# Kernel tuning notes

Measured on AMD Instinct MI355X. Metric: run time of the kernel, lower is better.

## Reference

```python
import jax, jax.numpy as jnp
import numpy as np

N, E, V, H, HEADS, L, B = 20000, 320000, 100, 128, 3, 2, 200
NEG = 0.2   # leaky_relu negative_slope
EPS = 1e-5  # LayerNorm eps


def _mean_nodes(x, gid):
    # dgl.mean_nodes: per-graph mean of node features
    s = jax.ops.segment_sum(x, gid, num_segments=B)
    c = jax.ops.segment_sum(jnp.ones((x.shape[0], 1), x.dtype), gid, num_segments=B)
    return s / jnp.maximum(c, 1.0)


def _gat_layer(h, src, dst, Wn, bn, att, Ws, b, gamma, beta):
    # weight_node: Linear(H, H*HEADS)
    wv = (h @ Wn + bn).reshape(-1, HEADS, H)
    u = wv[src]  # [E, heads, H] gathered src features
    # attn = leaky_relu(sum(cat(u, v) * w_att)) split into u/v halves (no concat materialized)
    attn = (jnp.einsum('ehd,hd->eh', u, att[:, :H])
            + jnp.einsum('ehd,hd->eh', wv[dst], att[:, H:]))
    attn = jax.nn.leaky_relu(attn, NEG)  # [E, heads]
    # segment softmax over incoming edges of each dst node (mailbox softmax)
    m = jax.ops.segment_max(attn, dst, num_segments=N)
    m = jnp.where(jnp.isfinite(m), m, 0.0)
    e = jnp.exp(attn - m[dst])
    s = jax.ops.segment_sum(e, dst, num_segments=N)
    score = e / s[dst]
    agg = jax.ops.segment_sum(score[:, :, None] * u, dst, num_segments=N)  # [N, heads, H]
    res = agg.reshape(-1, HEADS * H) @ Ws + b
    # DGL leaves zero-in-degree nodes with zero reduced features (reduce_func never runs)
    has_in = jax.ops.segment_sum(jnp.ones((E,), h.dtype), dst, num_segments=N) > 0
    res = jnp.where(has_in[:, None], res, 0.0)
    x = res + h  # residual, then LayerNorm, relu (dropout is eval-mode identity)
    mu = jnp.mean(x, -1, keepdims=True)
    var = jnp.var(x, -1, keepdims=True)
    x = (x - mu) * jax.lax.rsqrt(var + EPS) * gamma + beta
    return jax.nn.relu(x)


def _gru_dir(x, Wih, Whh, bih, bhh, reverse):
    # torch nn.GRU single direction; x: [B, T, in]
    def step(hprev, xt):
        gi = xt @ Wih.T + bih
        gh = hprev @ Whh.T + bhh
        ir, iz, inn = jnp.split(gi, 3, -1)
        hr, hz, hn = jnp.split(gh, 3, -1)
        r = jax.nn.sigmoid(ir + hr)
        z = jax.nn.sigmoid(iz + hz)
        n = jnp.tanh(inn + r * hn)
        hnew = (1.0 - z) * n + z * hprev
        return hnew, hnew
    h0 = jnp.zeros((x.shape[0], Whh.shape[1]), x.dtype)
    hT, ys = jax.lax.scan(step, h0, jnp.swapaxes(x, 0, 1), reverse=reverse)
    return jnp.swapaxes(ys, 0, 1), hT


def setup_inputs() -> dict:
    key = jax.random.key(0)
    k = jax.random.split(key, 16)
    sc = 0.05
    return {
        'h': jax.random.normal(k[0], (N, H), jnp.float32),
        'wid': jax.random.randint(k[1], (N,), 0, V),
        'src': jax.random.randint(k[2], (E,), 0, N),
        'dst': jax.random.randint(k[3], (E,), 0, N),
        'graph_ids': jnp.sort(jax.random.randint(k[4], (N,), 0, B)),
        'proj_W': jax.random.normal(k[5], (V + H, H), jnp.float32) * sc,
        'proj_b': jnp.zeros((H,), jnp.float32),
        'conv_Wn': jax.random.normal(k[6], (L, H, HEADS * H), jnp.float32) * sc,
        'conv_bn': jnp.zeros((L, HEADS * H), jnp.float32),
        'conv_att': jax.random.normal(k[7], (L, HEADS, 2 * H), jnp.float32) * sc,
        'conv_Ws': jax.random.normal(k[8], (L, HEADS * H, H), jnp.float32) * sc,
        'conv_b': jnp.zeros((L, H), jnp.float32),
        'conv_gamma': jnp.ones((L, H), jnp.float32),
        'conv_beta': jnp.zeros((L, H), jnp.float32),
        'gru_Wih0': jax.random.normal(k[9], (2, 3 * H, H), jnp.float32) * sc,
        'gru_Whh0': jax.random.normal(k[10], (2, 3 * H, H), jnp.float32) * sc,
        'gru_bih0': jnp.zeros((2, 3 * H), jnp.float32),
        'gru_bhh0': jnp.zeros((2, 3 * H), jnp.float32),
        'gru_Wih1': jax.random.normal(k[11], (2, 3 * H, 2 * H), jnp.float32) * sc,
        'gru_Whh1': jax.random.normal(k[12], (2, 3 * H, H), jnp.float32) * sc,
        'gru_bih1': jnp.zeros((2, 3 * H), jnp.float32),
        'gru_bhh1': jnp.zeros((2, 3 * H), jnp.float32),
    }


def reference(h, wid, src, dst, graph_ids, proj_W, proj_b, conv_Wn, conv_bn, conv_att, conv_Ws, conv_b, conv_gamma, conv_beta, gru_Wih0, gru_Whh0, gru_bih0, gru_bhh0, gru_Wih1, gru_Whh1, gru_bih1, gru_bhh1):
    one_hot = jax.nn.one_hot(wid, V, dtype=h.dtype)
    hcur = jnp.concatenate([one_hot, h], -1) @ proj_W + proj_b  # project
    readouts = [_mean_nodes(hcur, graph_ids)]
    for l in range(L):
        hcur = _gat_layer(hcur, src, dst, conv_Wn[l], conv_bn[l], conv_att[l],
                          conv_Ws[l], conv_b[l], conv_gamma[l], conv_beta[l])
        readouts.append(_mean_nodes(hcur, graph_ids))
    x = jnp.stack(readouts, 1)  # [B, L+1, H] GRU readout sequence
    finals = []
    for (Wih, Whh, bih, bhh) in ((gru_Wih0, gru_Whh0, gru_bih0, gru_bhh0),
                                 (gru_Wih1, gru_Whh1, gru_bih1, gru_bhh1)):
        yf, hf = _gru_dir(x, Wih[0], Whh[0], bih[0], bhh[0], False)
        yb, hb = _gru_dir(x, Wih[1], Whh[1], bih[1], bhh[1], True)
        x = jnp.concatenate([yf, yb], -1)
        finals += [hf, hb]
    # torch returns h_n [num_layers*2, B, H]; module takes mean over dim 0
    return jnp.mean(jnp.stack(finals, 0), 0)  # [B, H]
```

## Files before the change

### kernel.cpp

```cpp
#include <hip/hip_runtime.h>
#include <cstddef>
#include <cstdint>

static constexpr int Nn    = 20000;
static constexpr int Ee    = 320000;
static constexpr int Vv    = 100;
static constexpr int Hh    = 128;
static constexpr int HEADS = 3;
static constexpr int Bb    = 200;
static constexpr float NEG = 0.2f;
static constexpr float EPS = 1e-5f;

typedef short bf16x8 __attribute__((ext_vector_type(8)));
typedef float f32x4  __attribute__((ext_vector_type(4)));

__device__ inline unsigned short bf16_rne(float x) {
    unsigned u = __builtin_bit_cast(unsigned, x);
    u += 0x7FFFu + ((u >> 16) & 1u);
    return (unsigned short)(u >> 16);
}
__device__ inline float bf16_f(unsigned short h) {
    unsigned u = ((unsigned)h) << 16;
    return __builtin_bit_cast(float, u);
}
__device__ inline float bf_lo(unsigned u) { return __builtin_bit_cast(float, u << 16); }
__device__ inline float bf_hi(unsigned u) { return __builtin_bit_cast(float, u & 0xFFFF0000u); }
__device__ inline float lrelu(float a) { return a >= 0.f ? a : NEG * a; }
__device__ inline float sigmoidf(float x) { return 1.f / (1.f + __expf(-x)); }

__global__ __launch_bounds__(1024) void scan_offsets(const int* __restrict__ deg,
                                                     int* __restrict__ offs,
                                                     int* __restrict__ cur) {
    __shared__ int sums[1024];
    const int tid = threadIdx.x;
    const int per = (Nn + 1023) >> 10;
    int begin = tid * per;
    int end = begin + per; if (end > Nn) end = Nn;
    if (begin > Nn) begin = Nn;
    int s = 0;
    for (int i = begin; i < end; i++) s += deg[i];
    sums[tid] = s;
    __syncthreads();
    for (int off = 1; off < 1024; off <<= 1) {
        int v = (tid >= off) ? sums[tid - off] : 0;
        __syncthreads();
        sums[tid] += v;
        __syncthreads();
    }
    int run = sums[tid] - s;
    for (int i = begin; i < end; i++) {
        offs[i] = run; cur[i] = run;
        run += deg[i];
    }
    if (end == Nn) offs[Nn] = run;
}

__global__ void fill_csr(const int* __restrict__ dst, const int* __restrict__ src,
                         int* __restrict__ cur, int* __restrict__ csrc) {
    for (int i = blockIdx.x * blockDim.x + threadIdx.x; i < Ee; i += gridDim.x * blockDim.x) {
        int p = atomicAdd(&cur[dst[i]], 1);
        csrc[p] = src[i];
    }
}

struct PrepArgs {
    const float *projW, *convWn, *convWs, *convAtt, *convBn, *convB;
    const float *Wih0, *Whh0, *Wih1, *Whh1;
    const int *gid, *dst;
    unsigned short *pBth, *pBtl;
    unsigned short *WfTh0, *WfTl0, *WfTh1, *WfTl1;
    float *vavd, *vc, *biasF;
    float *WihT0, *WhhT0, *WihT1, *WhhT1;
    int *goffs, *deg;
};

__device__ inline void wsplit(const float* B, int K, int N, int idx,
                              unsigned short* Bth, unsigned short* Btl) {
    int k = idx / N, n = idx - k * N;
    float v = B[idx];
    unsigned short h = bf16_rne(v);
    unsigned short l = bf16_rne(v - bf16_f(h));
    Bth[(size_t)n * K + k] = h;
    Btl[(size_t)n * K + k] = l;
}
__device__ inline void gruT(const float* W, int K, int idx, float* WT) {
    int d = idx / (384 * K);
    int r = idx - d * 384 * K;
    int j = r / K, k = r - j * K;
    WT[(size_t)d * K * 384 + (size_t)(k >> 2) * 1536 + j * 4 + (k & 3)] = W[idx];
}

__global__ void prep_all(PrepArgs a) {
    int i = blockIdx.x * blockDim.x + threadIdx.x;
    if (i < 16384) { wsplit(a.projW, 128, 128, i, a.pBth, a.pBtl); return; } i -= 16384;
#pragma unroll
    for (int l = 0; l < 2; l++) {
        if (i < 49152) {
            int k = i >> 7, c = i & 127;
            int h = k >> 7, i_ = k & 127;
            const float* wn = a.convWn + (size_t)l * 49152 + (size_t)i_ * 384 + h * 128;
            const float* ws = a.convWs + (size_t)l * 49152 + (size_t)(h * 128) * 128 + c;
            float v = 0.f;
            for (int j = 0; j < 128; j++) v += wn[j] * ws[(size_t)j * 128];
            unsigned short hi = bf16_rne(v);
            unsigned short lo = bf16_rne(v - bf16_f(hi));
            unsigned short* th = l ? a.WfTh1 : a.WfTh0;
            unsigned short* tl = l ? a.WfTl1 : a.WfTl0;
            th[(size_t)c * 384 + k] = hi;
            tl[(size_t)c * 384 + k] = lo;
            return;
        }
        i -= 49152;
    }
    if (i < 1536) {
        int l = i / 768, r = i % 768;
        int sd = r / 384, rr = r % 384, h = rr >> 7, i_ = rr & 127;
        const float* wn = a.convWn + (size_t)l * 49152 + (size_t)i_ * 384 + h * 128;
        const float* at = a.convAtt + l * 768 + h * 256 + sd * 128;
        float v = 0.f;
        for (int j = 0; j < 128; j++) v += wn[j] * at[j];
        a.vavd[i] = v;
        return;
    } i -= 1536;
    if (i < 12) {
        int l = i / 6, r = i % 6, sd = r / 3, h = r % 3;
        const float* bn = a.convBn + l * 384 + h * 128;
        const float* at = a.convAtt + l * 768 + h * 256 + sd * 128;
        float v = 0.f;
        for (int j = 0; j < 128; j++) v += bn[j] * at[j];
        a.vc[i] = v;
        return;
    } i -= 12;
    if (i < 256) {
        int l = i >> 7, c = i & 127;
        const float* bn = a.convBn + l * 384;
        const float* ws = a.convWs + (size_t)l * 49152 + c;
        float v = a.convB[l * 128 + c];
        for (int k = 0; k < 384; k++) v += bn[k] * ws[(size_t)k * 128];
        a.biasF[i] = v;
        return;
    } i -= 256;
    if (i < 98304)  { gruT(a.Wih0, 128, i, a.WihT0); return; }  i -= 98304;
    if (i < 98304)  { gruT(a.Whh0, 128, i, a.WhhT0); return; }  i -= 98304;
    if (i < 196608) { gruT(a.Wih1, 256, i, a.WihT1); return; }  i -= 196608;
    if (i < 98304)  { gruT(a.Whh1, 128, i, a.WhhT1); return; }  i -= 98304;
    if (i < Nn) {
        int g = a.gid[i];
        if (i == 0) { for (int b = 0; b <= g; b++) a.goffs[b] = 0; }
        else { int pg = a.gid[i - 1]; for (int b = pg + 1; b <= g; b++) a.goffs[b] = i; }
        if (i == Nn - 1) { for (int b = g + 1; b <= Bb; b++) a.goffs[b] = Nn; }
        return;
    } i -= Nn;
    if (i < Ee) atomicAdd(&a.deg[a.dst[i]], 1);
}

struct GArgs {
    const float* A; const unsigned short* Bth; const unsigned short* Btl;
    const float* bias; int M, K;
    const int* wid; const float* projW;
    const int* deg; const float* gamma; const float* beta;
    float* hcur;
    const int* gid; float* reado;
    const float* vavd; const float* vc;
    float* adf; float* addf;
    unsigned short* hb;
};

template <int MODE>
__global__ __launch_bounds__(256) void gemm_fused(GArgs a) {
    __shared__ unsigned short As_hi[32][40];
    __shared__ unsigned short As_lo[32][40];
    __shared__ unsigned short Bs_hi[128][40];
    __shared__ unsigned short Bs_lo[128][40];
    __shared__ float ytile[32][132];
    __shared__ float sred[6][32][4];
    __shared__ int sgid[32];
    const int tid  = threadIdx.x;
    const int row0 = blockIdx.y * 32;
    const int wn   = tid >> 6;
    const int L    = tid & 63;
    const int lrow = L & 15;
    const int lq   = L >> 4;
    const int K = a.K;

    const int mA  = tid >> 3;
    const int kqA = (tid & 7) * 4;
    const int nB  = tid >> 1;
    const int khB = (tid & 1) * 16;
    const float* Arow = a.A + (size_t)(row0 + mA) * K + kqA;
    const unsigned short* Bhrow = a.Bth + (size_t)nB * K + khB;
    const unsigned short* Blrow = a.Btl + (size_t)nB * K + khB;

    f32x4 acc[2][2];
#pragma unroll
    for (int i = 0; i < 2; i++)
#pragma unroll
        for (int j = 0; j < 2; j++) acc[i][j] = (f32x4){0.f, 0.f, 0.f, 0.f};

    float4 av  = *(const float4*)(Arow);
    float4 vbh0 = *(const float4*)(Bhrow);
    float4 vbh1 = *(const float4*)(Bhrow + 8);
    float4 vbl0 = *(const float4*)(Blrow);
    float4 vbl1 = *(const float4*)(Blrow + 8);

    for (int kb = 0; kb < K; kb += 32) {
        {
            unsigned short h0 = bf16_rne(av.x), h1 = bf16_rne(av.y),
                           h2 = bf16_rne(av.z), h3 = bf16_rne(av.w);
            *(short4*)&As_hi[mA][kqA] = make_short4((short)h0, (short)h1, (short)h2, (short)h3);
            *(short4*)&As_lo[mA][kqA] = make_short4((short)bf16_rne(av.x - bf16_f(h0)),
                                                    (short)bf16_rne(av.y - bf16_f(h1)),
                                                    (short)bf16_rne(av.z - bf16_f(h2)),
                                                    (short)bf16_rne(av.w - bf16_f(h3)));
            *(float4*)&Bs_hi[nB][khB]     = vbh0;
            *(float4*)&Bs_hi[nB][khB + 8] = vbh1;
            *(float4*)&Bs_lo[nB][khB]     = vbl0;
            *(float4*)&Bs_lo[nB][khB + 8] = vbl1;
        }
        __syncthreads();
        if (kb + 32 < K) {
            av   = *(const float4*)(Arow + kb + 32);
            vbh0 = *(const float4*)(Bhrow + kb + 32);
            vbh1 = *(const float4*)(Bhrow + kb + 40);
            vbl0 = *(const float4*)(Blrow + kb + 32);
            vbl1 = *(const float4*)(Blrow + kb + 40);
        }
        bf16x8 ah[2], al[2], bh[2], bl[2];
#pragma unroll
        for (int mi = 0; mi < 2; mi++) {
            int r = mi * 16 + lrow;
            ah[mi] = *(const bf16x8*)&As_hi[r][lq * 8];
            al[mi] = *(const bf16x8*)&As_lo[r][lq * 8];
        }
#pragma unroll
        for (int ni = 0; ni < 2; ni++) {
            int r = wn * 32 + ni * 16 + lrow;
            bh[ni] = *(const bf16x8*)&Bs_hi[r][lq * 8];
            bl[ni] = *(const bf16x8*)&Bs_lo[r][lq * 8];
        }
#pragma unroll
        for (int mi = 0; mi < 2; mi++)
#pragma unroll
            for (int ni = 0; ni < 2; ni++) {
                acc[mi][ni] = __builtin_amdgcn_mfma_f32_16x16x32_bf16(ah[mi], bh[ni], acc[mi][ni], 0, 0, 0);
                acc[mi][ni] = __builtin_amdgcn_mfma_f32_16x16x32_bf16(ah[mi], bl[ni], acc[mi][ni], 0, 0, 0);
                acc[mi][ni] = __builtin_amdgcn_mfma_f32_16x16x32_bf16(al[mi], bh[ni], acc[mi][ni], 0, 0, 0);
            }
        __syncthreads();
    }

#pragma unroll
    for (int ni = 0; ni < 2; ni++) {
        float bb = a.bias[wn * 32 + ni * 16 + lrow];
#pragma unroll
        for (int mi = 0; mi < 2; mi++)
#pragma unroll
            for (int r = 0; r < 4; r++) acc[mi][ni][r] += bb;
    }

    if constexpr (MODE == 0) {
#pragma unroll
        for (int mi = 0; mi < 2; mi++)
#pragma unroll
            for (int r = 0; r < 4; r++) {
                int lr = mi * 16 + lq * 4 + r;
                int row = row0 + lr;
                int wi = a.wid[row];
#pragma unroll
                for (int ni = 0; ni < 2; ni++) {
                    int c = wn * 32 + ni * 16 + lrow;
                    float y = acc[mi][ni][r] + a.projW[(size_t)wi * 128 + c];
                    acc[mi][ni][r] = y;
                    a.hcur[(size_t)row * 128 + c] = y;
                    ytile[lr][c] = y;
                }
            }
    }

    if constexpr (MODE == 2) {
        __shared__ float red1[32][4], red2[32][4];
        float g4[2], be4[2];
#pragma unroll
        for (int ni = 0; ni < 2; ni++) {
            int c = wn * 32 + ni * 16 + lrow;
            g4[ni] = a.gamma[c]; be4[ni] = a.beta[c];
        }
#pragma unroll
        for (int mi = 0; mi < 2; mi++)
#pragma unroll
            for (int r = 0; r < 4; r++) {
                int lr = mi * 16 + lq * 4 + r;
                int row = row0 + lr;
                int dg = a.deg[row];
#pragma unroll
                for (int ni = 0; ni < 2; ni++) {
                    int c = wn * 32 + ni * 16 + lrow;
                    float hold = a.hcur[(size_t)row * 128 + c];
                    acc[mi][ni][r] = hold + (dg > 0 ? acc[mi][ni][r] : 0.f);
                }
            }
#pragma unroll
        for (int mi = 0; mi < 2; mi++)
#pragma unroll
            for (int r = 0; r < 4; r++) {
                float ps = acc[mi][0][r] + acc[mi][1][r];
#pragma unroll
                for (int o = 1; o < 16; o <<= 1) ps += __shfl_xor(ps, o, 64);
                if (lrow == 0) red1[mi * 16 + lq * 4 + r][wn] = ps;
            }
        __syncthreads();
#pragma unroll
        for (int mi = 0; mi < 2; mi++)
#pragma unroll
            for (int r = 0; r < 4; r++) {
                int lr = mi * 16 + lq * 4 + r;
                float mu = (red1[lr][0] + red1[lr][1] + red1[lr][2] + red1[lr][3]) * (1.f / 128.f);
                float qs = 0.f;
#pragma unroll
                for (int ni = 0; ni < 2; ni++) {
                    float dx = acc[mi][ni][r] - mu;
                    qs += dx * dx;
                }
#pragma unroll
                for (int o = 1; o < 16; o <<= 1) qs += __shfl_xor(qs, o, 64);
                if (lrow == 0) red2[lr][wn] = qs;
            }
        __syncthreads();
#pragma unroll
        for (int mi = 0; mi < 2; mi++)
#pragma unroll
            for (int r = 0; r < 4; r++) {
                int lr = mi * 16 + lq * 4 + r;
                int row = row0 + lr;
                float mu = (red1[lr][0] + red1[lr][1] + red1[lr][2] + red1[lr][3]) * (1.f / 128.f);
                float var = (red2[lr][0] + red2[lr][1] + red2[lr][2] + red2[lr][3]) * (1.f / 128.f);
                float rs = rsqrtf(var + EPS);
#pragma unroll
                for (int ni = 0; ni < 2; ni++) {
                    int c = wn * 32 + ni * 16 + lrow;
                    float y = fmaxf((acc[mi][ni][r] - mu) * rs * g4[ni] + be4[ni], 0.f);
                    acc[mi][ni][r] = y;
                    a.hcur[(size_t)row * 128 + c] = y;
                    ytile[lr][c] = y;
                }
            }
    }

    if (tid < 32) sgid[tid] = a.gid[row0 + tid];

    const bool dots = (a.vavd != nullptr);
    if (dots) {
        float vv0[6], vv1[6];
#pragma unroll
        for (int d = 0; d < 6; d++) {
            vv0[d] = a.vavd[d * 128 + wn * 32 + lrow];
            vv1[d] = a.vavd[d * 128 + wn * 32 + 16 + lrow];
        }
#pragma unroll
        for (int d = 0; d < 6; d++) {
#pragma unroll
            for (int mi = 0; mi < 2; mi++)
#pragma unroll
                for (int r = 0; r < 4; r++) {
                    float ps = acc[mi][0][r] * vv0[d] + acc[mi][1][r] * vv1[d];
#pragma unroll
                    for (int o = 1; o < 16; o <<= 1) ps += __shfl_xor(ps, o, 64);
                    if (lrow == 0) sred[d][mi * 16 + lq * 4 + r][wn] = ps;
                }
        }
    }
    __syncthreads();

    {
        int j = tid & 127, hh = tid >> 7;
        float sum = 0.f; int curg = -1;
        for (int r = hh * 16; r < hh * 16 + 16; r++) {
            int g = sgid[r];
            if (g != curg) {
                if (curg >= 0) atomicAdd(&a.reado[(size_t)curg * 128 + j], sum);
                sum = 0.f; curg = g;
            }
            sum += ytile[r][j];
        }
        if (curg >= 0) atomicAdd(&a.reado[(size_t)curg * 128 + j], sum);
    }

    if (dots) {
        if (tid < 192) {
            int row = tid & 31, d = tid >> 5;
            float s = sred[d][row][0] + sred[d][row][1] + sred[d][row][2] + sred[d][row][3]
                    + a.vc[d];
            int node = row0 + row;
            int sd = d / 3, h = d - sd * 3;
            float* dstp = sd ? a.addf : a.adf;
            dstp[(size_t)node * 4 + h] = s;
        }
        {
            int row = tid >> 3, c0 = (tid & 7) * 16;
            unsigned* dst = (unsigned*)(a.hb + (size_t)(row0 + row) * 128 + c0);
#pragma unroll
            for (int q = 0; q < 8; q++) {
                unsigned lo = bf16_rne(ytile[row][c0 + 2 * q]);
                unsigned hi = bf16_rne(ytile[row][c0 + 2 * q + 1]);
                dst[q] = lo | (hi << 16);
            }
        }
    }
}

__global__ __launch_bounds__(256) void gat_gather(const unsigned short* __restrict__ hb,
                                                  const float4* __restrict__ ad,
                                                  const float4* __restrict__ add,
                                                  const int* __restrict__ offs,
                                                  const int* __restrict__ csrc,
                                                  float* __restrict__ T) {
    __shared__ float4 slot[4][64];
    const int n = (blockIdx.x * 256 + threadIdx.x) >> 6;
    const int wv_ = threadIdx.x >> 6;
    const int L = threadIdx.x & 63;
    if (n >= Nn) return;
    const int start = offs[n];
    const int deg = offs[n + 1] - start;
    float2* o2 = (float2*)(T + (size_t)n * 384);
    if (deg == 0) {
        float2 z = make_float2(0.f, 0.f);
        o2[L] = z; o2[64 + L] = z; o2[128 + L] = z;
        return;
    }
    const float4 adn = add[n];
    float2 t0 = make_float2(0.f, 0.f), t1 = t0, t2 = t0;

    if (deg <= 64) {
        int sn = 0; float e0 = 0.f, e1 = 0.f, e2 = 0.f;
        if (L < deg) {
            sn = csrc[start + L];
            float4 a4 = ad[sn];
            e0 = __expf(lrelu(a4.x + adn.x));
            e1 = __expf(lrelu(a4.y + adn.y));
            e2 = __expf(lrelu(a4.z + adn.z));
        }
        float s0 = e0, s1 = e1, s2 = e2;
#pragma unroll
        for (int o = 32; o > 0; o >>= 1) {
            s0 += __shfl_xor(s0, o, 64);
            s1 += __shfl_xor(s1, o, 64);
            s2 += __shfl_xor(s2, o, 64);
        }
        slot[wv_][L] = make_float4(__builtin_bit_cast(float, sn),
                                   e0 / s0, e1 / s1, e2 / s2);
        __builtin_amdgcn_wave_barrier();
#pragma unroll 2
        for (int j = 0; j < deg; j++) {
            float4 sc = slot[wv_][j];
            int s_n = __builtin_bit_cast(int, sc.x);
            unsigned u = ((const unsigned*)(hb + (size_t)s_n * 128))[L];
            float x0 = bf_lo(u), x1 = bf_hi(u);
            t0.x += sc.y * x0; t0.y += sc.y * x1;
            t1.x += sc.z * x0; t1.y += sc.z * x1;
            t2.x += sc.w * x0; t2.y += sc.w * x1;
        }
    } else {
        float s0 = 0.f, s1 = 0.f, s2 = 0.f;
        for (int i = L; i < deg; i += 64) {
            int sn = csrc[start + i];
            float4 a4 = ad[sn];
            s0 += __expf(lrelu(a4.x + adn.x));
            s1 += __expf(lrelu(a4.y + adn.y));
            s2 += __expf(lrelu(a4.z + adn.z));
        }
#pragma unroll
        for (int o = 32; o > 0; o >>= 1) {
            s0 += __shfl_xor(s0, o, 64);
            s1 += __shfl_xor(s1, o, 64);
            s2 += __shfl_xor(s2, o, 64);
        }
        float i0 = 1.f / s0, i1 = 1.f / s1, i2 = 1.f / s2;
        for (int base = 0; base < deg; base += 64) {
            int cnt = deg - base; if (cnt > 64) cnt = 64;
            if (L < cnt) {
                int sn = csrc[start + base + L];
                float4 a4 = ad[sn];
                slot[wv_][L] = make_float4(__builtin_bit_cast(float, sn),
                                           __expf(lrelu(a4.x + adn.x)) * i0,
                                           __expf(lrelu(a4.y + adn.y)) * i1,
                                           __expf(lrelu(a4.z + adn.z)) * i2);
            }
            __builtin_amdgcn_wave_barrier();
            for (int j = 0; j < cnt; j++) {
                float4 sc = slot[wv_][j];
                int s_n = __builtin_bit_cast(int, sc.x);
                unsigned u = ((const unsigned*)(hb + (size_t)s_n * 128))[L];
                float x0 = bf_lo(u), x1 = bf_hi(u);
                t0.x += sc.y * x0; t0.y += sc.y * x1;
                t1.x += sc.z * x0; t1.y += sc.z * x1;
                t2.x += sc.w * x0; t2.y += sc.w * x1;
            }
            __builtin_amdgcn_wave_barrier();
        }
    }
    o2[L] = t0; o2[64 + L] = t1; o2[128 + L] = t2;
}

__global__ __launch_bounds__(768) void gru_all(const float* __restrict__ reado,
                                               const int* __restrict__ goffs,
                                               const float* __restrict__ WihT0,
                                               const float* __restrict__ WhhT0,
                                               const float* __restrict__ bih0,
                                               const float* __restrict__ bhh0,
                                               const float* __restrict__ WihT1,
                                               const float* __restrict__ WhhT1,
                                               const float* __restrict__ bih1,
                                               const float* __restrict__ bhh1,
                                               float* __restrict__ out) {
    const int b = blockIdx.x;
    const int tid = threadIdx.x;
    const int dir = tid / 384;
    const int j = tid - dir * 384;
    __shared__ __align__(16) float xs[3][128];
    __shared__ __align__(16) float y0s[3][256];
    __shared__ __align__(16) float hs[2][128];
    __shared__ float gil[2][384], ghl[2][384];
    __shared__ float fin01[2][128];
    if (tid < 128) {
        int cnt = goffs[b + 1] - goffs[b];
        float invc = 1.f / fmaxf((float)cnt, 1.f);
#pragma unroll
        for (int t = 0; t < 3; t++)
            xs[t][tid] = reado[(size_t)t * Bb * Hh + (size_t)b * Hh + tid] * invc;
    }
    if (j < 128) hs[dir][j] = 0.f;
    __syncthreads();
    {
        const float* Wi = WihT0 + (size_t)dir * 128 * 384;
        const float* Wh = WhhT0 + (size_t)dir * 128 * 384;
        float gi0, gi1, gi2;
        gi0 = gi1 = gi2 = bih0[dir * 384 + j];
#pragma unroll 4
        for (int k4 = 0; k4 < 32; k4++) {
            float4 w  = *(const float4*)(Wi + k4 * 1536 + j * 4);
            float4 x0 = *(const float4*)&xs[0][k4 * 4];
            float4 x1 = *(const float4*)&xs[1][k4 * 4];
            float4 x2 = *(const float4*)&xs[2][k4 * 4];
            gi0 += w.x * x0.x + w.y * x0.y + w.z * x0.z + w.w * x0.w;
            gi1 += w.x * x1.x + w.y * x1.y + w.z * x1.z + w.w * x1.w;
            gi2 += w.x * x2.x + w.y * x2.y + w.z * x2.z + w.w * x2.w;
        }
        const float bhj = bhh0[dir * 384 + j];
        for (int step = 0; step < 3; step++) {
            int t = dir ? 2 - step : step;
            float g = bhj;
            if (step > 0) {
#pragma unroll 4
                for (int k4 = 0; k4 < 32; k4++) {
                    float4 w  = *(const float4*)(Wh + k4 * 1536 + j * 4);
                    float4 hv = *(const float4*)&hs[dir][k4 * 4];
                    g += w.x * hv.x + w.y * hv.y + w.z * hv.z + w.w * hv.w;
                }
            }
            ghl[dir][j] = g;
            gil[dir][j] = dir ? (step == 0 ? gi2 : (step == 1 ? gi1 : gi0))
                              : (step == 0 ? gi0 : (step == 1 ? gi1 : gi2));
            __syncthreads();
            if (j < 128) {
                float r = sigmoidf(gil[dir][j] + ghl[dir][j]);
                float z = sigmoidf(gil[dir][j + 128] + ghl[dir][j + 128]);
                float nn2 = tanhf(gil[dir][j + 256] + r * ghl[dir][j + 256]);
                float hnew = (1.f - z) * nn2 + z * hs[dir][j];
                hs[dir][j] = hnew;
                y0s[t][dir * 128 + j] = hnew;
                if (step == 2) fin01[dir][j] = hnew;
            }
            __syncthreads();
        }
    }
    if (j < 128) hs[dir][j] = 0.f;
    {
        const float* Wi = WihT1 + (size_t)dir * 256 * 384;
        const float* Wh = WhhT1 + (size_t)dir * 128 * 384;
        float gi0, gi1, gi2;
        gi0 = gi1 = gi2 = bih1[dir * 384 + j];
        __syncthreads();
#pragma unroll 4
        for (int k4 = 0; k4 < 64; k4++) {
            float4 w  = *(const float4*)(Wi + k4 * 1536 + j * 4);
            float4 x0 = *(const float4*)&y0s[0][k4 * 4];
            float4 x1 = *(const float4*)&y0s[1][k4 * 4];
            float4 x2 = *(const float4*)&y0s[2][k4 * 4];
            gi0 += w.x * x0.x + w.y * x0.y + w.z * x0.z + w.w * x0.w;
            gi1 += w.x * x1.x + w.y * x1.y + w.z * x1.z + w.w * x1.w;
            gi2 += w.x * x2.x + w.y * x2.y + w.z * x2.z + w.w * x2.w;
        }
        const float bhj = bhh1[dir * 384 + j];
        for (int step = 0; step < 3; step++) {
            float g = bhj;
            if (step > 0) {
#pragma unroll 4
                for (int k4 = 0; k4 < 32; k4++) {
                    float4 w  = *(const float4*)(Wh + k4 * 1536 + j * 4);
                    float4 hv = *(const float4*)&hs[dir][k4 * 4];
                    g += w.x * hv.x + w.y * hv.y + w.z * hv.z + w.w * hv.w;
                }
            }
            ghl[dir][j] = g;
            gil[dir][j] = dir ? (step == 0 ? gi2 : (step == 1 ? gi1 : gi0))
                              : (step == 0 ? gi0 : (step == 1 ? gi1 : gi2));
            __syncthreads();
            if (j < 128) {
                float r = sigmoidf(gil[dir][j] + ghl[dir][j]);
                float z = sigmoidf(gil[dir][j + 128] + ghl[dir][j + 128]);
                float nn2 = tanhf(gil[dir][j + 256] + r * ghl[dir][j + 256]);
                float hnew = (1.f - z) * nn2 + z * hs[dir][j];
                hs[dir][j] = hnew;
                if (step == 2) fin01[dir][j] = 0.25f * (fin01[dir][j] + hnew);
            }
            __syncthreads();
        }
    }
    if (tid < 128)
        out[(size_t)b * Hh + tid] = fin01[0][tid] + fin01[1][tid];
}

extern "C" void kernel_launch(void* const* d_in, const int* in_sizes, int n_in,
                              void* d_out, int out_size, void* d_ws, size_t ws_size,
                              hipStream_t stream) {
    const float* h      = (const float*)d_in[0];
    const int*   wid    = (const int*)d_in[1];
    const int*   src    = (const int*)d_in[2];
    const int*   dst    = (const int*)d_in[3];
    const int*   gid    = (const int*)d_in[4];
    const float* projW  = (const float*)d_in[5];
    const float* projB  = (const float*)d_in[6];
    const float* convWn = (const float*)d_in[7];
    const float* convBn = (const float*)d_in[8];
    const float* convAtt= (const float*)d_in[9];
    const float* convWs = (const float*)d_in[10];
    const float* convB  = (const float*)d_in[11];
    const float* convG  = (const float*)d_in[12];
    const float* convBe = (const float*)d_in[13];
    const float* Wih0   = (const float*)d_in[14];
    const float* Whh0   = (const float*)d_in[15];
    const float* bih0   = (const float*)d_in[16];
    const float* bhh0   = (const float*)d_in[17];
    const float* Wih1   = (const float*)d_in[18];
    const float* Whh1   = (const float*)d_in[19];
    const float* bih1   = (const float*)d_in[20];
    const float* bhh1   = (const float*)d_in[21];
    float* out = (float*)d_out;

    char* p = (char*)d_ws;
    auto align16 = [&]() { p = (char*)(((uintptr_t)p + 15) & ~(uintptr_t)15); };
    auto alloc_f = [&](size_t n) { align16(); float* r = (float*)p; p += n * sizeof(float); return r; };
    auto alloc_i = [&](size_t n) { align16(); int* r = (int*)p; p += n * sizeof(int); return r; };
    auto alloc_s = [&](size_t n) { align16(); unsigned short* r = (unsigned short*)p; p += n * sizeof(unsigned short); return r; };
    float* hcur  = alloc_f((size_t)Nn * 128);
    float* T     = alloc_f((size_t)Nn * 384);
    float* adbuf = alloc_f((size_t)Nn * 4);
    float* addbuf= alloc_f((size_t)Nn * 4);
    float* reado = alloc_f((size_t)3 * Bb * Hh);
    int* deg  = alloc_i(Nn);
    const size_t zero_bytes = (size_t)3 * Bb * Hh * sizeof(float) + Nn * sizeof(int);
    float* WihT0 = alloc_f((size_t)2 * 128 * 384);
    float* WhhT0 = alloc_f((size_t)2 * 128 * 384);
    float* WihT1 = alloc_f((size_t)2 * 256 * 384);
    float* WhhT1 = alloc_f((size_t)2 * 128 * 384);
    float* vavd  = alloc_f(1536);
    float* vc    = alloc_f(12);
    float* biasF = alloc_f(256);
    int* offs = alloc_i(Nn + 1);
    int* cur  = alloc_i(Nn);
    int* csrc = alloc_i(Ee);
    int* goffs = alloc_i(Bb + 1);
    unsigned short* hb = alloc_s((size_t)Nn * 128);
    unsigned short* pBth = alloc_s(128 * 128);
    unsigned short* pBtl = alloc_s(128 * 128);
    unsigned short* WfTh[2] = { alloc_s(128 * 384), alloc_s(128 * 384) };
    unsigned short* WfTl[2] = { alloc_s(128 * 384), alloc_s(128 * 384) };

    hipMemsetAsync(reado, 0, zero_bytes, stream);

    PrepArgs pa;
    pa.projW = projW + (size_t)Vv * Hh;
    pa.convWn = convWn; pa.convWs = convWs; pa.convAtt = convAtt;
    pa.convBn = convBn; pa.convB = convB;
    pa.Wih0 = Wih0; pa.Whh0 = Whh0; pa.Wih1 = Wih1; pa.Whh1 = Whh1;
    pa.gid = gid; pa.dst = dst;
    pa.pBth = pBth; pa.pBtl = pBtl;
    pa.WfTh0 = WfTh[0]; pa.WfTl0 = WfTl[0]; pa.WfTh1 = WfTh[1]; pa.WfTl1 = WfTl[1];
    pa.vavd = vavd; pa.vc = vc; pa.biasF = biasF;
    pa.WihT0 = WihT0; pa.WhhT0 = WhhT0; pa.WihT1 = WihT1; pa.WhhT1 = WhhT1;
    pa.goffs = goffs; pa.deg = deg;
    const int prep_total = 16384 + 2 * 49152 + 1536 + 12 + 256 + 98304 + 98304 + 196608 + 98304 + Nn + Ee;
    prep_all<<<(prep_total + 255) / 256, 256, 0, stream>>>(pa);

    scan_offsets<<<1, 1024, 0, stream>>>(deg, offs, cur);
    fill_csr<<<1250, 256, 0, stream>>>(dst, src, cur, csrc);

    {
        GArgs g = {};
        g.A = h; g.Bth = pBth; g.Btl = pBtl; g.bias = projB;
        g.M = Nn; g.K = 128;
        g.wid = wid; g.projW = projW; g.hcur = hcur;
        g.gid = gid; g.reado = reado;
        g.vavd = vavd; g.vc = vc; g.adf = adbuf; g.addf = addbuf; g.hb = hb;
        gemm_fused<0><<<dim3(1, Nn / 32), 256, 0, stream>>>(g);
    }

    const int nwaveblocks = (Nn * 64 + 255) / 256;
    for (int l = 0; l < 2; l++) {
        gat_gather<<<nwaveblocks, 256, 0, stream>>>(hb, (const float4*)adbuf, (const float4*)addbuf,
                                                    offs, csrc, T);
        {
            GArgs g = {};
            g.A = T; g.Bth = WfTh[l]; g.Btl = WfTl[l]; g.bias = biasF + l * 128;
            g.M = Nn; g.K = 384;
            g.deg = deg; g.gamma = convG + l * Hh; g.beta = convBe + l * Hh;
            g.hcur = hcur;
            g.gid = gid; g.reado = reado + (size_t)(l + 1) * Bb * Hh;
            if (l == 0) { g.vavd = vavd + 768; g.vc = vc + 6; g.adf = adbuf; g.addf = addbuf; g.hb = hb; }
            gemm_fused<2><<<dim3(1, Nn / 32), 256, 0, stream>>>(g);
        }
    }

    gru_all<<<Bb, 768, 0, stream>>>(reado, goffs, WihT0, WhhT0, bih0, bhh0,
                                    WihT1, WhhT1, bih1, bhh1, out);
}
```

Before: 349.8 us.

## Fuse memset, prep, scan and CSR fill into one cooperative kernel

Replaces the memset, prep kernel, single-block scan and CSR fill kernels with one cooperative-launch kernel that uses grid-wide syncs between phases. The goal is to remove several launch and inter-kernel gaps. The cost is grid.sync overhead and a smaller grid of 1024 blocks striding over the prep work. The scan now runs on a 256-thread block inside a single block while the rest of the grid sits idle at the barrier, so that serial phase may take longer.

```diff
diff --git a/kernel.cpp b/kernel.cpp
--- a/kernel.cpp
+++ b/kernel.cpp
@@ -1,6 +1,9 @@
 #include <hip/hip_runtime.h>
+#include <hip/hip_cooperative_groups.h>
 #include <cstddef>
 #include <cstdint>
+
+namespace cg = cooperative_groups;
 
 static constexpr int Nn    = 20000;
 static constexpr int Ee    = 320000;
@@ -28,50 +31,17 @@
 __device__ inline float lrelu(float a) { return a >= 0.f ? a : NEG * a; }
 __device__ inline float sigmoidf(float x) { return 1.f / (1.f + __expf(-x)); }
 
-__global__ __launch_bounds__(1024) void scan_offsets(const int* __restrict__ deg,
-                                                     int* __restrict__ offs,
-                                                     int* __restrict__ cur) {
-    __shared__ int sums[1024];
-    const int tid = threadIdx.x;
-    const int per = (Nn + 1023) >> 10;
-    int begin = tid * per;
-    int end = begin + per; if (end > Nn) end = Nn;
-    if (begin > Nn) begin = Nn;
-    int s = 0;
-    for (int i = begin; i < end; i++) s += deg[i];
-    sums[tid] = s;
-    __syncthreads();
-    for (int off = 1; off < 1024; off <<= 1) {
-        int v = (tid >= off) ? sums[tid - off] : 0;
-        __syncthreads();
-        sums[tid] += v;
-        __syncthreads();
-    }
-    int run = sums[tid] - s;
-    for (int i = begin; i < end; i++) {
-        offs[i] = run; cur[i] = run;
-        run += deg[i];
-    }
-    if (end == Nn) offs[Nn] = run;
-}
-
-__global__ void fill_csr(const int* __restrict__ dst, const int* __restrict__ src,
-                         int* __restrict__ cur, int* __restrict__ csrc) {
-    for (int i = blockIdx.x * blockDim.x + threadIdx.x; i < Ee; i += gridDim.x * blockDim.x) {
-        int p = atomicAdd(&cur[dst[i]], 1);
-        csrc[p] = src[i];
-    }
-}
-
 struct PrepArgs {
     const float *projW, *convWn, *convWs, *convAtt, *convBn, *convB;
     const float *Wih0, *Whh0, *Wih1, *Whh1;
-    const int *gid, *dst;
+    const int *gid, *dst, *src;
     unsigned short *pBth, *pBtl;
     unsigned short *WfTh0, *WfTl0, *WfTh1, *WfTl1;
     float *vavd, *vc, *biasF;
     float *WihT0, *WhhT0, *WihT1, *WhhT1;
     int *goffs, *deg;
+    int *offs, *cur, *csrc;
+    float *reado;
 };
 
 __device__ inline void wsplit(const float* B, int K, int N, int idx,
@@ -90,8 +60,10 @@
     WT[(size_t)d * K * 384 + (size_t)(k >> 2) * 1536 + j * 4 + (k & 3)] = W[idx];
 }
 
-__global__ void prep_all(PrepArgs a) {
-    int i = blockIdx.x * blockDim.x + threadIdx.x;
+static constexpr int PREP_TOTAL = 16384 + 2 * 49152 + 1536 + 12 + 256
+                                + 98304 + 98304 + 196608 + 98304 + Nn + Ee;
+
+__device__ void prep_item(const PrepArgs& a, int i) {
     if (i < 16384) { wsplit(a.projW, 128, 128, i, a.pBth, a.pBtl); return; } i -= 16384;
 #pragma unroll
     for (int l = 0; l < 2; l++) {
@@ -154,6 +126,50 @@
     if (i < Ee) atomicAdd(&a.deg[a.dst[i]], 1);
 }
 
+__global__ __launch_bounds__(256) void prep_fused(PrepArgs a) {
+    cg::grid_group grid = cg::this_grid();
+    const int gsz  = gridDim.x * blockDim.x;
+    const int gtid = blockIdx.x * blockDim.x + threadIdx.x;
+    const int tid  = threadIdx.x;
+
+    for (int i = gtid; i < Nn; i += gsz) a.deg[i] = 0;
+    for (int i = gtid; i < 3 * Bb * Hh; i += gsz) a.reado[i] = 0.f;
+    grid.sync();
+
+    for (int i = gtid; i < PREP_TOTAL; i += gsz) prep_item(a, i);
+    grid.sync();
+
+    if (blockIdx.x == 0) {
+        __shared__ int sums[256];
+        const int per = (Nn + 255) >> 8;
+        int begin = tid * per;
+        int end = begin + per; if (end > Nn) end = Nn;
+        if (begin > Nn) begin = Nn;
+        int s = 0;
+        for (int i = begin; i < end; i++) s += a.deg[i];
+        sums[tid] = s;
+        __syncthreads();
+        for (int off = 1; off < 256; off <<= 1) {
+            int v = (tid >= off) ? sums[tid - off] : 0;
+            __syncthreads();
+            sums[tid] += v;
+            __syncthreads();
+        }
+        int run = sums[tid] - s;
+        for (int i = begin; i < end; i++) {
+            a.offs[i] = run; a.cur[i] = run;
+            run += a.deg[i];
+        }
+        if (end == Nn) a.offs[Nn] = run;
+    }
+    grid.sync();
+
+    for (int i = gtid; i < Ee; i += gsz) {
+        int p = atomicAdd(&a.cur[a.dst[i]], 1);
+        a.csrc[p] = a.src[i];
+    }
+}
+
 struct GArgs {
     const float* A; const unsigned short* Bth; const unsigned short* Btl;
     const float* bias; int M, K;
@@ -658,7 +674,6 @@
     float* addbuf= alloc_f((size_t)Nn * 4);
     float* reado = alloc_f((size_t)3 * Bb * Hh);
     int* deg  = alloc_i(Nn);
-    const size_t zero_bytes = (size_t)3 * Bb * Hh * sizeof(float) + Nn * sizeof(int);
     float* WihT0 = alloc_f((size_t)2 * 128 * 384);
     float* WhhT0 = alloc_f((size_t)2 * 128 * 384);
     float* WihT1 = alloc_f((size_t)2 * 256 * 384);
@@ -676,24 +691,25 @@
     unsigned short* WfTh[2] = { alloc_s(128 * 384), alloc_s(128 * 384) };
     unsigned short* WfTl[2] = { alloc_s(128 * 384), alloc_s(128 * 384) };
 
-    hipMemsetAsync(reado, 0, zero_bytes, stream);
-
     PrepArgs pa;
     pa.projW = projW + (size_t)Vv * Hh;
     pa.convWn = convWn; pa.convWs = convWs; pa.convAtt = convAtt;
     pa.convBn = convBn; pa.convB = convB;
     pa.Wih0 = Wih0; pa.Whh0 = Whh0; pa.Wih1 = Wih1; pa.Whh1 = Whh1;
-    pa.gid = gid; pa.dst = dst;
+    pa.gid = gid; pa.dst = dst; pa.src = src;
     pa.pBth = pBth; pa.pBtl = pBtl;
     pa.WfTh0 = WfTh[0]; pa.WfTl0 = WfTl[0]; pa.WfTh1 = WfTh[1]; pa.WfTl1 = WfTl[1];
     pa.vavd = vavd; pa.vc = vc; pa.biasF = biasF;
     pa.WihT0 = WihT0; pa.WhhT0 = WhhT0; pa.WihT1 = WihT1; pa.WhhT1 = WhhT1;
     pa.goffs = goffs; pa.deg = deg;
-    const int prep_total = 16384 + 2 * 49152 + 1536 + 12 + 256 + 98304 + 98304 + 196608 + 98304 + Nn + Ee;
-    prep_all<<<(prep_total + 255) / 256, 256, 0, stream>>>(pa);
-
-    scan_offsets<<<1, 1024, 0, stream>>>(deg, offs, cur);
-    fill_csr<<<1250, 256, 0, stream>>>(dst, src, cur, csrc);
+    pa.offs = offs; pa.cur = cur; pa.csrc = csrc;
+    pa.reado = reado;
+
+    {
+        void* kargs[] = { (void*)&pa };
+        hipLaunchCooperativeKernel((void*)prep_fused, dim3(1024), dim3(256),
+                                   kargs, 0, stream);
+    }
 
     {
         GArgs g = {};
```

After: 723.7 us. +106.9%, slower.
